# Optimization experiments

Hardware: AMD Instinct MI355X
Metric: run time of the kernel (lower is better)

## Reference

```python
import jax, jax.numpy as jnp
import numpy as np

FIELD = 7  # field_size


def _conv1x1(x, w):
    # x: [b,c,h,w], w: [c_out,c_in] (1x1 conv, no bias)
    return jnp.einsum('bchw,oc->bohw', x, w)


def _patches(x, f):
    # torch unfold with 'same' padding: output [b, c*f*f, h, w], channel-major
    # (feature index = c*f*f + kh*f + kw), matching KAIR extract_image_patches
    # layout for odd f / stride 1 (symmetric pad (f-1)//2).
    return jax.lax.conv_general_dilated_patches(
        x, filter_shape=(f, f), window_strides=(1, 1), padding='SAME',
        dimension_numbers=('NCHW', 'OIHW', 'NCHW'))


def setup_inputs() -> dict:
    key = jax.random.key(0)
    k0, k1, k2, k3, k4 = jax.random.split(key, 5)
    c, ci = 256, 128
    b, h, w = 4, 64, 64
    s = 1.0 / np.sqrt(c)
    si = 1.0 / np.sqrt(ci)
    return {
        'x': jax.random.normal(k0, (b, c, h, w), dtype=jnp.float32),
        'w_phi': jax.random.normal(k1, (ci, c), dtype=jnp.float32) * s,
        'w_theta': jax.random.normal(k2, (ci, c), dtype=jnp.float32) * s,
        'w_g': jax.random.normal(k3, (ci, c), dtype=jnp.float32) * s,
        'w_mask': jax.random.normal(k4, (c, ci), dtype=jnp.float32) * si,
    }


def reference(x, w_phi, w_theta, w_g, w_mask):
    b, c, h, w = x.shape
    ci = w_phi.shape[0]
    f = FIELD
    kk = f * f

    x_phi = _conv1x1(x, w_phi)      # [b,ci,h,w]
    x_g = _conv1x1(x, w_g)          # [b,ci,h,w]
    x_theta = _conv1x1(x, w_theta)  # [b,ci,h,w]

    # theta: unsqueeze(-2) then permute(0,2,4,3,1) -> [b,h,w,1,ci]
    q = jnp.transpose(x_theta, (0, 2, 3, 1))[:, :, :, None, :]

    # phi patches: [b, ci*kk, h, w] reshaped (row-major, faithful to torch
    # reshape of the unfold output) to [b,h,w,ci,kk]
    p_phi = _patches(x_phi, f).reshape(b, h, w, ci, kk)
    scores = jnp.matmul(q, p_phi)                 # [b,h,w,1,kk]
    attn = jax.nn.softmax(scores, axis=1)         # softmax over dim=1 (h), faithful

    p_g = _patches(x_g, f).reshape(b, h, w, kk, ci)
    out = jnp.matmul(attn, p_g)                   # [b,h,w,1,ci]

    # permute(0,4,3,1,2).view(b,ci,h,w)
    y = jnp.transpose(out, (0, 4, 3, 1, 2)).reshape(b, ci, h, w)
    mask = _conv1x1(y, w_mask)                    # [b,c,h,w]
    return mask + x
```

## Files before the change

### kernel.cpp

```cpp
#include <hip/hip_runtime.h>


#define PLANE    5040
#define A_BATCH  645120

typedef __attribute__((ext_vector_type(8))) short short8;
typedef __attribute__((ext_vector_type(4))) float floatx4;

__device__ __forceinline__ float bf2f(unsigned short u) {
    union { unsigned int i; float f; } v; v.i = ((unsigned int)u) << 16; return v.f;
}
__device__ __forceinline__ unsigned short f2bf(float f) {
    union { float f; unsigned int i; } v; v.f = f;
    unsigned int r = v.i + 0x7FFFu + ((v.i >> 16) & 1u);
    return (unsigned short)(r >> 16);
}

__global__ __launch_bounds__(256) void prep_kernel(
    const float* __restrict__ x,
    const float* __restrict__ w_phi,
    const float* __restrict__ w_theta,
    const float* __restrict__ w_g,
    const float* __restrict__ w_mask,
    unsigned short* __restrict__ xp_hi,
    unsigned short* __restrict__ xp_lo,
    unsigned short* __restrict__ w3p_hi,
    unsigned short* __restrict__ w3p_lo,
    unsigned short* __restrict__ wmp_hi,
    unsigned short* __restrict__ wmp_lo,
    uint4* __restrict__ zero_region)
{
    const int tid = threadIdx.x;
    const int bx = blockIdx.x;

    if (bx < 1024) {
        const int b  = bx >> 8;
        const int kt = (bx >> 6) & 3;
        const int pt = bx & 63;
        __shared__ float tile[64][65];
        #pragma unroll
        for (int i = 0; i < 16; ++i) {
            int lin = tid + i * 256;
            int kk = lin >> 6, pp = lin & 63;
            tile[kk][pp] = x[(b * 256 + kt * 64 + kk) * 4096 + pt * 64 + pp];
        }
        __syncthreads();
        #pragma unroll
        for (int i = 0; i < 16; ++i) {
            int lin = tid + i * 256;
            int frag = lin >> 9;
            int idx  = lin & 511;
            int kbL  = frag >> 2;
            int ptL  = frag & 3;
            int j    = idx & 7;
            int n    = (idx >> 3) & 15;
            int quad = idx >> 7;
            float f = tile[kbL * 32 + quad * 8 + j][ptL * 16 + n];
            unsigned short h = f2bf(f);
            int addr = ((b * 8 + kt * 2 + kbL) * 256 + pt * 4 + ptL) * 512 + idx;
            xp_hi[addr] = h;
            xp_lo[addr] = f2bf(f - bf2f(h));
        }
    } else {
        const int wid = (bx - 1024) * 256 + tid;
        for (int e = wid; e < 98304; e += 32768) {
            int frag = e >> 9;
            int idx  = e & 511;
            int nt16 = frag >> 3, kb = frag & 7;
            int j = idx & 7, m = (idx >> 3) & 15, quad = idx >> 7;
            int n = nt16 * 16 + m;
            int k = kb * 32 + quad * 8 + j;
            float v = (n < 128) ? w_phi[n * 256 + k]
                    : (n < 256) ? w_theta[(n - 128) * 256 + k]
                                : w_g[(n - 256) * 256 + k];
            unsigned short h = f2bf(v);
            w3p_hi[e] = h;
            w3p_lo[e] = f2bf(v - bf2f(h));
        }
        {
            int e = wid;
            int frag = e >> 9;
            int idx  = e & 511;
            int ot16 = frag >> 2, kb = frag & 3;
            int j = idx & 7, m = (idx >> 3) & 15, quad = idx >> 7;
            float v = w_mask[(ot16 * 16 + m) * 128 + kb * 32 + quad * 8 + j];
            unsigned short h = f2bf(v);
            wmp_hi[e] = h;
            wmp_lo[e] = f2bf(v - bf2f(h));
        }
        const uint4 z = make_uint4(0u, 0u, 0u, 0u);
        for (int i = wid; i < 645120; i += 32768) zero_region[i] = z;
    }
}

__global__ __launch_bounds__(256) void conv3_mfma_kernel(
    const unsigned short* __restrict__ xp_hi,
    const unsigned short* __restrict__ xp_lo,
    const unsigned short* __restrict__ w3p_hi,
    const unsigned short* __restrict__ w3p_lo,
    unsigned short* __restrict__ A_phi,
    unsigned short* __restrict__ theta_bf,
    unsigned short* __restrict__ A_g)
{
    const int tid = threadIdx.x;
    const int w   = tid >> 6;
    const int ln  = tid & 63;
    const int lm  = ln & 15;
    const int quad = ln >> 4;
    const int bx = blockIdx.x;
    const int nt = blockIdx.y;
    const int b  = blockIdx.z;
    const int nt16 = nt * 4 + w;
    const int lnofs = ln * 8;

    floatx4 acc0 = {0.f, 0.f, 0.f, 0.f};
    floatx4 acc1 = {0.f, 0.f, 0.f, 0.f};
    floatx4 acc2 = {0.f, 0.f, 0.f, 0.f};
    floatx4 acc3 = {0.f, 0.f, 0.f, 0.f};

    #pragma unroll
    for (int kb = 0; kb < 8; ++kb) {
        const int aoff = (nt16 * 8 + kb) * 512 + lnofs;
        const int boff = ((b * 8 + kb) * 256 + bx * 4) * 512 + lnofs;
        short8 ah = *reinterpret_cast<const short8*>(w3p_hi + aoff);
        short8 al = *reinterpret_cast<const short8*>(w3p_lo + aoff);
        short8 bh0 = *reinterpret_cast<const short8*>(xp_hi + boff);
        short8 bh1 = *reinterpret_cast<const short8*>(xp_hi + boff + 512);
        short8 bh2 = *reinterpret_cast<const short8*>(xp_hi + boff + 1024);
        short8 bh3 = *reinterpret_cast<const short8*>(xp_hi + boff + 1536);
        short8 bl0 = *reinterpret_cast<const short8*>(xp_lo + boff);
        short8 bl1 = *reinterpret_cast<const short8*>(xp_lo + boff + 512);
        short8 bl2 = *reinterpret_cast<const short8*>(xp_lo + boff + 1024);
        short8 bl3 = *reinterpret_cast<const short8*>(xp_lo + boff + 1536);
        acc0 = __builtin_amdgcn_mfma_f32_16x16x32_bf16(ah, bh0, acc0, 0, 0, 0);
        acc1 = __builtin_amdgcn_mfma_f32_16x16x32_bf16(ah, bh1, acc1, 0, 0, 0);
        acc2 = __builtin_amdgcn_mfma_f32_16x16x32_bf16(ah, bh2, acc2, 0, 0, 0);
        acc3 = __builtin_amdgcn_mfma_f32_16x16x32_bf16(ah, bh3, acc3, 0, 0, 0);
        acc0 = __builtin_amdgcn_mfma_f32_16x16x32_bf16(ah, bl0, acc0, 0, 0, 0);
        acc1 = __builtin_amdgcn_mfma_f32_16x16x32_bf16(ah, bl1, acc1, 0, 0, 0);
        acc2 = __builtin_amdgcn_mfma_f32_16x16x32_bf16(ah, bl2, acc2, 0, 0, 0);
        acc3 = __builtin_amdgcn_mfma_f32_16x16x32_bf16(ah, bl3, acc3, 0, 0, 0);
        acc0 = __builtin_amdgcn_mfma_f32_16x16x32_bf16(al, bh0, acc0, 0, 0, 0);
        acc1 = __builtin_amdgcn_mfma_f32_16x16x32_bf16(al, bh1, acc1, 0, 0, 0);
        acc2 = __builtin_amdgcn_mfma_f32_16x16x32_bf16(al, bh2, acc2, 0, 0, 0);
        acc3 = __builtin_amdgcn_mfma_f32_16x16x32_bf16(al, bh3, acc3, 0, 0, 0);
    }

    floatx4 accs[4] = {acc0, acc1, acc2, acc3};
    const int n0 = nt16 * 16;
    const int py = bx;
    if (nt == 2 || nt == 3) {
        #pragma unroll
        for (int ct = 0; ct < 4; ++ct) {
            const int p = bx * 64 + ct * 16 + lm;
            #pragma unroll
            for (int reg = 0; reg < 4; ++reg) {
                const int n = n0 + quad * 4 + reg;
                theta_bf[(b * 4096 + p) * 128 + (n - 128)] = f2bf(accs[ct][reg]);
            }
        }
    } else {
        unsigned short* __restrict__ A = (nt < 2) ? A_phi : A_g;
        const int nbias = (nt < 2) ? 0 : 256;
        #pragma unroll
        for (int ct = 0; ct < 4; ++ct) {
            const int pxx = ct * 16 + lm;
            #pragma unroll
            for (int reg = 0; reg < 4; ++reg) {
                const int pl = n0 + quad * 4 + reg - nbias;
                A[b * A_BATCH + pl * PLANE + (py + 3) * 72 + pxx + 4] =
                    f2bf(accs[ct][reg]);
            }
        }
    }
}

__global__ __launch_bounds__(256) void scores_kernel(
    const unsigned short* __restrict__ Apad,
    const unsigned short* __restrict__ theta_bf,
    float* __restrict__ scores)
{
    const int w  = threadIdx.x >> 6;
    const int ln = threadIdx.x & 63;
    const int s  = blockIdx.x * 4 + w;
    const int b  = blockIdx.y;

    __shared__ float th[4][128];
    {
        const unsigned short* tb = theta_bf + (b * 4096 + s) * 128;
        th[w][ln]      = bf2f(tb[ln]);
        th[w][ln + 64] = bf2f(tb[ln + 64]);
    }
    __syncthreads();

    const unsigned short* __restrict__ Ab = Apad + b * A_BATCH;

    const int base  = s * 6272;
    const int ch_lo = base >> 12;
    const unsigned B1 = (unsigned)(ch_lo + 1) << 12;
    const unsigned B2 = (unsigned)(ch_lo + 2) << 12;
    const int d1 = (int)B1 - base;
    const int d2 = d1 + 4096;

    int A1 = d1 / 49;
    int A2 = (d1 + 48) / 49;
    int C1 = d2 / 49;        if (C1 > 128) C1 = 128;
    int C2 = (d2 + 48) / 49; if (C2 > 128) C2 = 128;

    unsigned OFFv[3];
    #pragma unroll
    for (int i = 0; i < 3; ++i) {
        int ch = ch_lo + i;
        int c0 = ch / 49; if (c0 > 127) c0 = 127;
        int rr = ch - c0 * 49;
        int kh = rr / 7;
        int kw = rr - kh * 7;
        OFFv[i] = (unsigned)(c0 * PLANE + kh * 72 + kw + 1);
    }

    unsigned F = (unsigned)(base + ln);
    float acc = 0.f;

    {
        const unsigned OFF_ = OFFv[0];
        #pragma unroll 4
        for (int cc = 0; cc < A1; ++cc) {
            unsigned p = F & 4095u;
            unsigned a = OFF_ + p + ((p >> 6) << 3);
            acc = fmaf(th[w][cc], bf2f(Ab[a]), acc);
            F += 49u;
        }
    }
    for (int cc = A1; cc < A2; ++cc) {
        unsigned OFF_ = (F >= B1) ? OFFv[1] : OFFv[0];
        unsigned p = F & 4095u;
        unsigned a = OFF_ + p + ((p >> 6) << 3);
        acc = fmaf(th[w][cc], bf2f(Ab[a]), acc);
        F += 49u;
    }
    {
        const unsigned OFF_ = OFFv[1];
        #pragma unroll 4
        for (int cc = A2; cc < C1; ++cc) {
            unsigned p = F & 4095u;
            unsigned a = OFF_ + p + ((p >> 6) << 3);
            acc = fmaf(th[w][cc], bf2f(Ab[a]), acc);
            F += 49u;
        }
    }
    for (int cc = C1; cc < C2; ++cc) {
        unsigned OFF_ = (F >= B2) ? OFFv[2] : OFFv[1];
        unsigned p = F & 4095u;
        unsigned a = OFF_ + p + ((p >> 6) << 3);
        acc = fmaf(th[w][cc], bf2f(Ab[a]), acc);
        F += 49u;
    }
    {
        const unsigned OFF_ = OFFv[2];
        #pragma unroll 4
        for (int cc = C2; cc < 128; ++cc) {
            unsigned p = F & 4095u;
            unsigned a = OFF_ + p + ((p >> 6) << 3);
            acc = fmaf(th[w][cc], bf2f(Ab[a]), acc);
            F += 49u;
        }
    }

    if (ln < 49) scores[(b * 4096 + s) * 64 + ln] = acc;
}

__global__ __launch_bounds__(256) void softmax_kernel(float* __restrict__ scores)
{
    const int b = blockIdx.x >> 6;
    const int j = blockIdx.x & 63;
    const int tid = threadIdx.x;
    const int wv = tid >> 6;
    const int ln = tid & 63;

    __shared__ float tile[64][52];
    __shared__ float inv[52];

    #pragma unroll
    for (int it = 0; it < 16; ++it) {
        int i = it * 4 + wv;
        if (ln < 49) tile[i][ln] = scores[(b * 4096 + i * 64 + j) * 64 + ln];
    }
    __syncthreads();

    if (tid < 49) {
        float m = -3.4e38f;
        #pragma unroll 8
        for (int i = 0; i < 64; ++i) m = fmaxf(m, tile[i][tid]);
        float sum = 0.f;
        #pragma unroll 8
        for (int i = 0; i < 64; ++i) {
            float e = __expf(tile[i][tid] - m);
            tile[i][tid] = e;
            sum += e;
        }
        inv[tid] = 1.f / sum;
    }
    __syncthreads();

    #pragma unroll
    for (int it = 0; it < 16; ++it) {
        int i = it * 4 + wv;
        if (ln < 49) scores[(b * 4096 + i * 64 + j) * 64 + ln] = tile[i][ln] * inv[ln];
    }
}

__global__ __launch_bounds__(256) void aggregate_kernel(
    const float* __restrict__ scores,
    const unsigned short* __restrict__ Apad,
    unsigned short* __restrict__ y_p)
{
    const int pix = threadIdx.x >> 7;
    const int cc  = threadIdx.x & 127;
    const int s   = blockIdx.x * 2 + pix;
    const int b   = blockIdx.y;

    __shared__ float at[2][52];
    if (cc < 49) at[pix][cc] = scores[(b * 4096 + s) * 64 + cc];
    __syncthreads();

    const unsigned short* __restrict__ Ab = Apad + b * A_BATCH;

    const int base  = s * 6272;
    const int ch_lo = base >> 12;
    const unsigned B1 = (unsigned)(ch_lo + 1) << 12;
    const unsigned B2 = (unsigned)(ch_lo + 2) << 12;
    const int d1 = (int)B1 - base;
    const int d2 = d1 + 4096;

    int A1 = d1 >> 7;
    int A2 = (d1 + 127) >> 7;
    int C1 = d2 >> 7;          if (C1 > 49) C1 = 49;
    int C2 = (d2 + 127) >> 7;  if (C2 > 49) C2 = 49;
    if (A1 > 49) A1 = 49;
    if (A2 > 49) A2 = 49;

    unsigned OFFv[3];
    #pragma unroll
    for (int i = 0; i < 3; ++i) {
        int ch = ch_lo + i;
        int c0 = ch / 49; if (c0 > 127) c0 = 127;
        int rr = ch - c0 * 49;
        int kh = rr / 7;
        int kw = rr - kh * 7;
        OFFv[i] = (unsigned)(c0 * PLANE + kh * 72 + kw + 1);
    }

    unsigned F = (unsigned)(base + cc);
    float acc = 0.f;

    {
        const unsigned OFF_ = OFFv[0];
        #pragma unroll 4
        for (int t = 0; t < A1; ++t) {
            unsigned p = F & 4095u;
            unsigned a = OFF_ + p + ((p >> 6) << 3);
            acc = fmaf(at[pix][t], bf2f(Ab[a]), acc);
            F += 128u;
        }
    }
    for (int t = A1; t < A2; ++t) {
        unsigned OFF_ = (F >= B1) ? OFFv[1] : OFFv[0];
        unsigned p = F & 4095u;
        unsigned a = OFF_ + p + ((p >> 6) << 3);
        acc = fmaf(at[pix][t], bf2f(Ab[a]), acc);
        F += 128u;
    }
    {
        const unsigned OFF_ = OFFv[1];
        #pragma unroll 4
        for (int t = A2; t < C1; ++t) {
            unsigned p = F & 4095u;
            unsigned a = OFF_ + p + ((p >> 6) << 3);
            acc = fmaf(at[pix][t], bf2f(Ab[a]), acc);
            F += 128u;
        }
    }
    for (int t = C1; t < C2; ++t) {
        unsigned OFF_ = (F >= B2) ? OFFv[2] : OFFv[1];
        unsigned p = F & 4095u;
        unsigned a = OFF_ + p + ((p >> 6) << 3);
        acc = fmaf(at[pix][t], bf2f(Ab[a]), acc);
        F += 128u;
    }
    {
        const unsigned OFF_ = OFFv[2];
        for (int t = C2; t < 49; ++t) {
            unsigned p = F & 4095u;
            unsigned a = OFF_ + p + ((p >> 6) << 3);
            acc = fmaf(at[pix][t], bf2f(Ab[a]), acc);
            F += 128u;
        }
    }

    const int kb = cc >> 5, k32 = cc & 31;
    const int quad = k32 >> 3, j = k32 & 7;
    const int pt16 = s >> 4, n = s & 15;
    y_p[((b * 4 + kb) * 256 + pt16) * 512 + (quad * 16 + n) * 8 + j] = f2bf(acc);
}

__global__ __launch_bounds__(256) void maskconv_mfma_kernel(
    const float* __restrict__ x,
    const unsigned short* __restrict__ wmp_hi,
    const unsigned short* __restrict__ wmp_lo,
    const unsigned short* __restrict__ y_p,
    float* __restrict__ out)
{
    const int tid = threadIdx.x;
    const int w   = tid >> 6;
    const int ln  = tid & 63;
    const int lm  = ln & 15;
    const int quad = ln >> 4;
    const int bx = blockIdx.x;
    const int ot = blockIdx.y;
    const int b  = blockIdx.z;
    const int ot16 = ot * 4 + w;
    const int lnofs = ln * 8;

    floatx4 acc0 = {0.f, 0.f, 0.f, 0.f};
    floatx4 acc1 = {0.f, 0.f, 0.f, 0.f};
    floatx4 acc2 = {0.f, 0.f, 0.f, 0.f};
    floatx4 acc3 = {0.f, 0.f, 0.f, 0.f};

    #pragma unroll
    for (int kb = 0; kb < 4; ++kb) {
        const int aoff = (ot16 * 4 + kb) * 512 + lnofs;
        const int boff = ((b * 4 + kb) * 256 + bx * 4) * 512 + lnofs;
        short8 ah = *reinterpret_cast<const short8*>(wmp_hi + aoff);
        short8 al = *reinterpret_cast<const short8*>(wmp_lo + aoff);
        short8 b0 = *reinterpret_cast<const short8*>(y_p + boff);
        short8 b1 = *reinterpret_cast<const short8*>(y_p + boff + 512);
        short8 b2 = *reinterpret_cast<const short8*>(y_p + boff + 1024);
        short8 b3 = *reinterpret_cast<const short8*>(y_p + boff + 1536);
        acc0 = __builtin_amdgcn_mfma_f32_16x16x32_bf16(ah, b0, acc0, 0, 0, 0);
        acc1 = __builtin_amdgcn_mfma_f32_16x16x32_bf16(ah, b1, acc1, 0, 0, 0);
        acc2 = __builtin_amdgcn_mfma_f32_16x16x32_bf16(ah, b2, acc2, 0, 0, 0);
        acc3 = __builtin_amdgcn_mfma_f32_16x16x32_bf16(ah, b3, acc3, 0, 0, 0);
        acc0 = __builtin_amdgcn_mfma_f32_16x16x32_bf16(al, b0, acc0, 0, 0, 0);
        acc1 = __builtin_amdgcn_mfma_f32_16x16x32_bf16(al, b1, acc1, 0, 0, 0);
        acc2 = __builtin_amdgcn_mfma_f32_16x16x32_bf16(al, b2, acc2, 0, 0, 0);
        acc3 = __builtin_amdgcn_mfma_f32_16x16x32_bf16(al, b3, acc3, 0, 0, 0);
    }

    floatx4 accs[4] = {acc0, acc1, acc2, acc3};
    const int o0 = ot16 * 16;
    #pragma unroll
    for (int ct = 0; ct < 4; ++ct) {
        const int p = bx * 64 + ct * 16 + lm;
        #pragma unroll
        for (int reg = 0; reg < 4; ++reg) {
            const int o = o0 + quad * 4 + reg;
            const int ofs = (b * 256 + o) * 4096 + p;
            out[ofs] = accs[ct][reg] + x[ofs];
        }
    }
}

extern "C" void kernel_launch(void* const* d_in, const int* in_sizes, int n_in,
                              void* d_out, int out_size, void* d_ws, size_t ws_size,
                              hipStream_t stream) {
    const float* x       = (const float*)d_in[0];
    const float* w_phi   = (const float*)d_in[1];
    const float* w_theta = (const float*)d_in[2];
    const float* w_g     = (const float*)d_in[3];
    const float* w_mask  = (const float*)d_in[4];

    float* out_f = (float*)d_out;

    unsigned short* ws_u  = (unsigned short*)d_ws;
    unsigned short* A_phi = ws_u;
    unsigned short* A_g   = ws_u + 2580480;
    unsigned short* y_p   = ws_u + 5160960;
    unsigned short* th_u  = ws_u + 7258112;
    float*          sc_f  = (float*)(ws_u + 9355264);
    unsigned short* xph   = ws_u + 11452416;
    unsigned short* xpl   = ws_u + 15646720;
    unsigned short* w3ph  = ws_u + 19841024;
    unsigned short* w3pl  = ws_u + 19939328;
    unsigned short* wmph  = ws_u + 20037632;
    unsigned short* wmpl  = ws_u + 20070400;

    hipLaunchKernelGGL(prep_kernel, dim3(1152), dim3(256), 0, stream,
                       x, w_phi, w_theta, w_g, w_mask,
                       xph, xpl, w3ph, w3pl, wmph, wmpl, (uint4*)A_phi);
    hipLaunchKernelGGL(conv3_mfma_kernel, dim3(64, 6, 4), dim3(256), 0, stream,
                       xph, xpl, w3ph, w3pl, A_phi, th_u, A_g);
    hipLaunchKernelGGL(scores_kernel, dim3(1024, 4), dim3(256), 0, stream,
                       A_phi, th_u, sc_f);
    hipLaunchKernelGGL(softmax_kernel, dim3(256), dim3(256), 0, stream, sc_f);
    hipLaunchKernelGGL(aggregate_kernel, dim3(2048, 4), dim3(256), 0, stream,
                       sc_f, A_g, y_p);
    hipLaunchKernelGGL(maskconv_mfma_kernel, dim3(64, 4, 4), dim3(256), 0, stream,
                       x, wmph, wmpl, y_p, out_f);
}
```

Before: 181.9 us.

## Double output tiles per wave in 1x1 convs and fold softmax normalize into aggregate

Each wave in the conv3 and mask-conv MFMA kernels now computes two 16-row output tiles that share the same B-operand loads. This halves the grid and the redundant activation loads, at the cost of twice the accumulator registers. The softmax kernel now writes only per-column max and inverse-sum statistics instead of rewriting the normalized scores. The aggregate kernel applies exp and the scale on the fly, which removes one full read-modify-write pass over the scores buffer.

```diff
diff --git a/kernel.cpp b/kernel.cpp
--- a/kernel.cpp
+++ b/kernel.cpp
@@ -110,66 +110,65 @@
     const int bx = blockIdx.x;
     const int nt = blockIdx.y;
     const int b  = blockIdx.z;
-    const int nt16 = nt * 4 + w;
+    const int nt16a = nt * 8 + w;
+    const int nt16b = nt * 8 + 4 + w;
     const int lnofs = ln * 8;
 
-    floatx4 acc0 = {0.f, 0.f, 0.f, 0.f};
-    floatx4 acc1 = {0.f, 0.f, 0.f, 0.f};
-    floatx4 acc2 = {0.f, 0.f, 0.f, 0.f};
-    floatx4 acc3 = {0.f, 0.f, 0.f, 0.f};
+    floatx4 accA[4] = {{0.f,0.f,0.f,0.f},{0.f,0.f,0.f,0.f},
+                       {0.f,0.f,0.f,0.f},{0.f,0.f,0.f,0.f}};
+    floatx4 accB[4] = {{0.f,0.f,0.f,0.f},{0.f,0.f,0.f,0.f},
+                       {0.f,0.f,0.f,0.f},{0.f,0.f,0.f,0.f}};
 
     #pragma unroll
     for (int kb = 0; kb < 8; ++kb) {
-        const int aoff = (nt16 * 8 + kb) * 512 + lnofs;
-        const int boff = ((b * 8 + kb) * 256 + bx * 4) * 512 + lnofs;
-        short8 ah = *reinterpret_cast<const short8*>(w3p_hi + aoff);
-        short8 al = *reinterpret_cast<const short8*>(w3p_lo + aoff);
-        short8 bh0 = *reinterpret_cast<const short8*>(xp_hi + boff);
-        short8 bh1 = *reinterpret_cast<const short8*>(xp_hi + boff + 512);
-        short8 bh2 = *reinterpret_cast<const short8*>(xp_hi + boff + 1024);
-        short8 bh3 = *reinterpret_cast<const short8*>(xp_hi + boff + 1536);
-        short8 bl0 = *reinterpret_cast<const short8*>(xp_lo + boff);
-        short8 bl1 = *reinterpret_cast<const short8*>(xp_lo + boff + 512);
-        short8 bl2 = *reinterpret_cast<const short8*>(xp_lo + boff + 1024);
-        short8 bl3 = *reinterpret_cast<const short8*>(xp_lo + boff + 1536);
-        acc0 = __builtin_amdgcn_mfma_f32_16x16x32_bf16(ah, bh0, acc0, 0, 0, 0);
-        acc1 = __builtin_amdgcn_mfma_f32_16x16x32_bf16(ah, bh1, acc1, 0, 0, 0);
-        acc2 = __builtin_amdgcn_mfma_f32_16x16x32_bf16(ah, bh2, acc2, 0, 0, 0);
-        acc3 = __builtin_amdgcn_mfma_f32_16x16x32_bf16(ah, bh3, acc3, 0, 0, 0);
-        acc0 = __builtin_amdgcn_mfma_f32_16x16x32_bf16(ah, bl0, acc0, 0, 0, 0);
-        acc1 = __builtin_amdgcn_mfma_f32_16x16x32_bf16(ah, bl1, acc1, 0, 0, 0);
-        acc2 = __builtin_amdgcn_mfma_f32_16x16x32_bf16(ah, bl2, acc2, 0, 0, 0);
-        acc3 = __builtin_amdgcn_mfma_f32_16x16x32_bf16(ah, bl3, acc3, 0, 0, 0);
-        acc0 = __builtin_amdgcn_mfma_f32_16x16x32_bf16(al, bh0, acc0, 0, 0, 0);
-        acc1 = __builtin_amdgcn_mfma_f32_16x16x32_bf16(al, bh1, acc1, 0, 0, 0);
-        acc2 = __builtin_amdgcn_mfma_f32_16x16x32_bf16(al, bh2, acc2, 0, 0, 0);
-        acc3 = __builtin_amdgcn_mfma_f32_16x16x32_bf16(al, bh3, acc3, 0, 0, 0);
-    }
-
-    floatx4 accs[4] = {acc0, acc1, acc2, acc3};
-    const int n0 = nt16 * 16;
+        const int aoffA = (nt16a * 8 + kb) * 512 + lnofs;
+        const int aoffB = (nt16b * 8 + kb) * 512 + lnofs;
+        const int boff  = ((b * 8 + kb) * 256 + bx * 4) * 512 + lnofs;
+        short8 ahA = *reinterpret_cast<const short8*>(w3p_hi + aoffA);
+        short8 alA = *reinterpret_cast<const short8*>(w3p_lo + aoffA);
+        short8 ahB = *reinterpret_cast<const short8*>(w3p_hi + aoffB);
+        short8 alB = *reinterpret_cast<const short8*>(w3p_lo + aoffB);
+        short8 bh[4], bl[4];
+        #pragma unroll
+        for (int ct = 0; ct < 4; ++ct) {
+            bh[ct] = *reinterpret_cast<const short8*>(xp_hi + boff + ct * 512);
+            bl[ct] = *reinterpret_cast<const short8*>(xp_lo + boff + ct * 512);
+        }
+        #pragma unroll
+        for (int ct = 0; ct < 4; ++ct) {
+            accA[ct] = __builtin_amdgcn_mfma_f32_16x16x32_bf16(ahA, bh[ct], accA[ct], 0, 0, 0);
+            accA[ct] = __builtin_amdgcn_mfma_f32_16x16x32_bf16(ahA, bl[ct], accA[ct], 0, 0, 0);
+            accA[ct] = __builtin_amdgcn_mfma_f32_16x16x32_bf16(alA, bh[ct], accA[ct], 0, 0, 0);
+            accB[ct] = __builtin_amdgcn_mfma_f32_16x16x32_bf16(ahB, bh[ct], accB[ct], 0, 0, 0);
+            accB[ct] = __builtin_amdgcn_mfma_f32_16x16x32_bf16(ahB, bl[ct], accB[ct], 0, 0, 0);
+            accB[ct] = __builtin_amdgcn_mfma_f32_16x16x32_bf16(alB, bh[ct], accB[ct], 0, 0, 0);
+        }
+    }
+
     const int py = bx;
-    if (nt == 2 || nt == 3) {
+    if (nt == 1) {
         #pragma unroll
         for (int ct = 0; ct < 4; ++ct) {
             const int p = bx * 64 + ct * 16 + lm;
             #pragma unroll
             for (int reg = 0; reg < 4; ++reg) {
-                const int n = n0 + quad * 4 + reg;
-                theta_bf[(b * 4096 + p) * 128 + (n - 128)] = f2bf(accs[ct][reg]);
+                const int r = w * 16 + quad * 4 + reg;
+                theta_bf[(b * 4096 + p) * 128 + r]      = f2bf(accA[ct][reg]);
+                theta_bf[(b * 4096 + p) * 128 + r + 64] = f2bf(accB[ct][reg]);
             }
         }
     } else {
-        unsigned short* __restrict__ A = (nt < 2) ? A_phi : A_g;
-        const int nbias = (nt < 2) ? 0 : 256;
+        unsigned short* __restrict__ A = (nt == 0) ? A_phi : A_g;
         #pragma unroll
         for (int ct = 0; ct < 4; ++ct) {
             const int pxx = ct * 16 + lm;
             #pragma unroll
             for (int reg = 0; reg < 4; ++reg) {
-                const int pl = n0 + quad * 4 + reg - nbias;
-                A[b * A_BATCH + pl * PLANE + (py + 3) * 72 + pxx + 4] =
-                    f2bf(accs[ct][reg]);
+                const int r = w * 16 + quad * 4 + reg;
+                A[b * A_BATCH + r * PLANE + (py + 3) * 72 + pxx + 4] =
+                    f2bf(accA[ct][reg]);
+                A[b * A_BATCH + (r + 64) * PLANE + (py + 3) * 72 + pxx + 4] =
+                    f2bf(accB[ct][reg]);
             }
         }
     }
@@ -269,7 +268,10 @@
     if (ln < 49) scores[(b * 4096 + s) * 64 + ln] = acc;
 }
 
-__global__ __launch_bounds__(256) void softmax_kernel(float* __restrict__ scores)
+__global__ __launch_bounds__(256) void softmax_stats_kernel(
+    const float* __restrict__ scores,
+    float* __restrict__ m_arr,
+    float* __restrict__ inv_arr)
 {
     const int b = blockIdx.x >> 6;
     const int j = blockIdx.x & 63;
@@ -278,7 +280,6 @@
     const int ln = tid & 63;
 
     __shared__ float tile[64][52];
-    __shared__ float inv[52];
 
     #pragma unroll
     for (int it = 0; it < 16; ++it) {
@@ -293,24 +294,16 @@
         for (int i = 0; i < 64; ++i) m = fmaxf(m, tile[i][tid]);
         float sum = 0.f;
         #pragma unroll 8
-        for (int i = 0; i < 64; ++i) {
-            float e = __expf(tile[i][tid] - m);
-            tile[i][tid] = e;
-            sum += e;
-        }
-        inv[tid] = 1.f / sum;
-    }
-    __syncthreads();
-
-    #pragma unroll
-    for (int it = 0; it < 16; ++it) {
-        int i = it * 4 + wv;
-        if (ln < 49) scores[(b * 4096 + i * 64 + j) * 64 + ln] = tile[i][ln] * inv[ln];
+        for (int i = 0; i < 64; ++i) sum += __expf(tile[i][tid] - m);
+        m_arr[(b * 64 + j) * 49 + tid]   = m;
+        inv_arr[(b * 64 + j) * 49 + tid] = 1.f / sum;
     }
 }
 
 __global__ __launch_bounds__(256) void aggregate_kernel(
     const float* __restrict__ scores,
+    const float* __restrict__ m_arr,
+    const float* __restrict__ inv_arr,
     const unsigned short* __restrict__ Apad,
     unsigned short* __restrict__ y_p)
 {
@@ -320,7 +313,13 @@
     const int b   = blockIdx.y;
 
     __shared__ float at[2][52];
-    if (cc < 49) at[pix][cc] = scores[(b * 4096 + s) * 64 + cc];
+    if (cc < 49) {
+        const int j = s & 63;
+        float sc = scores[(b * 4096 + s) * 64 + cc];
+        float m  = m_arr[(b * 64 + j) * 49 + cc];
+        float iv = inv_arr[(b * 64 + j) * 49 + cc];
+        at[pix][cc] = __expf(sc - m) * iv;
+    }
     __syncthreads();
 
     const unsigned short* __restrict__ Ab = Apad + b * A_BATCH;
@@ -418,44 +417,47 @@
     const int bx = blockIdx.x;
     const int ot = blockIdx.y;
     const int b  = blockIdx.z;
-    const int ot16 = ot * 4 + w;
+    const int ot16a = ot * 8 + w;
+    const int ot16b = ot * 8 + 4 + w;
     const int lnofs = ln * 8;
 
-    floatx4 acc0 = {0.f, 0.f, 0.f, 0.f};
-    floatx4 acc1 = {0.f, 0.f, 0.f, 0.f};
-    floatx4 acc2 = {0.f, 0.f, 0.f, 0.f};
-    floatx4 acc3 = {0.f, 0.f, 0.f, 0.f};
+    floatx4 accA[4] = {{0.f,0.f,0.f,0.f},{0.f,0.f,0.f,0.f},
+                       {0.f,0.f,0.f,0.f},{0.f,0.f,0.f,0.f}};
+    floatx4 accB[4] = {{0.f,0.f,0.f,0.f},{0.f,0.f,0.f,0.f},
+                       {0.f,0.f,0.f,0.f},{0.f,0.f,0.f,0.f}};
 
     #pragma unroll
     for (int kb = 0; kb < 4; ++kb) {
-        const int aoff = (ot16 * 4 + kb) * 512 + lnofs;
-        const int boff = ((b * 4 + kb) * 256 + bx * 4) * 512 + lnofs;
-        short8 ah = *reinterpret_cast<const short8*>(wmp_hi + aoff);
-        short8 al = *reinterpret_cast<const short8*>(wmp_lo + aoff);
-        short8 b0 = *reinterpret_cast<const short8*>(y_p + boff);
-        short8 b1 = *reinterpret_cast<const short8*>(y_p + boff + 512);
-        short8 b2 = *reinterpret_cast<const short8*>(y_p + boff + 1024);
-        short8 b3 = *reinterpret_cast<const short8*>(y_p + boff + 1536);
-        acc0 = __builtin_amdgcn_mfma_f32_16x16x32_bf16(ah, b0, acc0, 0, 0, 0);
-        acc1 = __builtin_amdgcn_mfma_f32_16x16x32_bf16(ah, b1, acc1, 0, 0, 0);
-        acc2 = __builtin_amdgcn_mfma_f32_16x16x32_bf16(ah, b2, acc2, 0, 0, 0);
-        acc3 = __builtin_amdgcn_mfma_f32_16x16x32_bf16(ah, b3, acc3, 0, 0, 0);
-        acc0 = __builtin_amdgcn_mfma_f32_16x16x32_bf16(al, b0, acc0, 0, 0, 0);
-        acc1 = __builtin_amdgcn_mfma_f32_16x16x32_bf16(al, b1, acc1, 0, 0, 0);
-        acc2 = __builtin_amdgcn_mfma_f32_16x16x32_bf16(al, b2, acc2, 0, 0, 0);
-        acc3 = __builtin_amdgcn_mfma_f32_16x16x32_bf16(al, b3, acc3, 0, 0, 0);
-    }
-
-    floatx4 accs[4] = {acc0, acc1, acc2, acc3};
-    const int o0 = ot16 * 16;
+        const int aoffA = (ot16a * 4 + kb) * 512 + lnofs;
+        const int aoffB = (ot16b * 4 + kb) * 512 + lnofs;
+        const int boff  = ((b * 4 + kb) * 256 + bx * 4) * 512 + lnofs;
+        short8 ahA = *reinterpret_cast<const short8*>(wmp_hi + aoffA);
+        short8 alA = *reinterpret_cast<const short8*>(wmp_lo + aoffA);
+        short8 ahB = *reinterpret_cast<const short8*>(wmp_hi + aoffB);
+        short8 alB = *reinterpret_cast<const short8*>(wmp_lo + aoffB);
+        short8 bf[4];
+        #pragma unroll
+        for (int ct = 0; ct < 4; ++ct)
+            bf[ct] = *reinterpret_cast<const short8*>(y_p + boff + ct * 512);
+        #pragma unroll
+        for (int ct = 0; ct < 4; ++ct) {
+            accA[ct] = __builtin_amdgcn_mfma_f32_16x16x32_bf16(ahA, bf[ct], accA[ct], 0, 0, 0);
+            accA[ct] = __builtin_amdgcn_mfma_f32_16x16x32_bf16(alA, bf[ct], accA[ct], 0, 0, 0);
+            accB[ct] = __builtin_amdgcn_mfma_f32_16x16x32_bf16(ahB, bf[ct], accB[ct], 0, 0, 0);
+            accB[ct] = __builtin_amdgcn_mfma_f32_16x16x32_bf16(alB, bf[ct], accB[ct], 0, 0, 0);
+        }
+    }
+
     #pragma unroll
     for (int ct = 0; ct < 4; ++ct) {
         const int p = bx * 64 + ct * 16 + lm;
         #pragma unroll
         for (int reg = 0; reg < 4; ++reg) {
-            const int o = o0 + quad * 4 + reg;
-            const int ofs = (b * 256 + o) * 4096 + p;
-            out[ofs] = accs[ct][reg] + x[ofs];
+            const int oA = ot * 128 + w * 16 + quad * 4 + reg;
+            const int ofsA = (b * 256 + oA) * 4096 + p;
+            out[ofsA] = accA[ct][reg] + x[ofsA];
+            const int ofsB = ofsA + 64 * 4096;
+            out[ofsB] = accB[ct][reg] + x[ofsB];
         }
     }
 }
@@ -483,17 +485,20 @@
     unsigned short* w3pl  = ws_u + 19939328;
     unsigned short* wmph  = ws_u + 20037632;
     unsigned short* wmpl  = ws_u + 20070400;
+    float*          m_f   = (float*)(ws_u + 20103168);
+    float*          inv_f = (float*)(ws_u + 20128256);
 
     hipLaunchKernelGGL(prep_kernel, dim3(1152), dim3(256), 0, stream,
                        x, w_phi, w_theta, w_g, w_mask,
                        xph, xpl, w3ph, w3pl, wmph, wmpl, (uint4*)A_phi);
-    hipLaunchKernelGGL(conv3_mfma_kernel, dim3(64, 6, 4), dim3(256), 0, stream,
+    hipLaunchKernelGGL(conv3_mfma_kernel, dim3(64, 3, 4), dim3(256), 0, stream,
                        xph, xpl, w3ph, w3pl, A_phi, th_u, A_g);
     hipLaunchKernelGGL(scores_kernel, dim3(1024, 4), dim3(256), 0, stream,
                        A_phi, th_u, sc_f);
-    hipLaunchKernelGGL(softmax_kernel, dim3(256), dim3(256), 0, stream, sc_f);
+    hipLaunchKernelGGL(softmax_stats_kernel, dim3(256), dim3(256), 0, stream,
+                       sc_f, m_f, inv_f);
     hipLaunchKernelGGL(aggregate_kernel, dim3(2048, 4), dim3(256), 0, stream,
-                       sc_f, A_g, y_p);
-    hipLaunchKernelGGL(maskconv_mfma_kernel, dim3(64, 4, 4), dim3(256), 0, stream,
+                       sc_f, m_f, inv_f, A_g, y_p);
+    hipLaunchKernelGGL(maskconv_mfma_kernel, dim3(64, 2, 4), dim3(256), 0, stream,
                        x, wmph, wmpl, y_p, out_f);
 }
```

New measurement: 176.8 us. 2.8% less time.
